# Kernel optimization log

Hardware: AMD Instinct MI355X
Metric: run time of the kernel (lower is better)

Reference implementation:

```python
import jax, jax.numpy as jnp
import numpy as np

B, L, IN_DIM = 1024, 2048, 64
ATT_DIM, H, TOPK = 64, 4, 64
D = ATT_DIM // H  # head_dim = 16
SCALE = D ** 0.5


def setup_inputs() -> dict:
    key = jax.random.key(0)
    k1, k2, k3, k4, k5, k6, k7 = jax.random.split(key, 7)
    return {
        "target_item": jax.random.normal(k1, (B, IN_DIM), dtype=jnp.float32),
        "item_sequence": jax.random.normal(k2, (B, L, IN_DIM), dtype=jnp.float32),
        "mask": jax.random.randint(k3, (B, L), 0, 2, dtype=jnp.int32),
        # Linear weights stored as (in, out); x @ W == torch Linear(x)
        "W_q": jax.random.normal(k4, (IN_DIM, ATT_DIM), dtype=jnp.float32) * 0.05,
        "W_h": jax.random.normal(k5, (IN_DIM, ATT_DIM), dtype=jnp.float32) * 0.05,
        "W_v": jax.random.normal(k6, (IN_DIM, ATT_DIM), dtype=jnp.float32) * 0.05,
        "W_o": jax.random.normal(k7, (ATT_DIM, IN_DIM), dtype=jnp.float32) * 0.05,
    }


def reference(target_item, item_sequence, mask, W_q, W_h, W_v, W_o):
    b = target_item.shape[0]
    # Projections (Kc == 0 path: item_feat_seq == item_sequence)
    q = (target_item @ W_q).reshape(b, H, D)          # b h d (single query)
    k = (item_sequence @ W_h).reshape(b, L, H, D)      # b l h d
    v = (item_sequence @ W_v).reshape(b, L, H, D)      # b l h d

    scores = jnp.einsum("bhd,blhd->bhl", q, k) / SCALE  # b h l
    scores = jnp.where(mask[:, None, :] == 0, jnp.float32(-1e9), scores)

    topk_scores, topk_idx = jax.lax.top_k(scores, TOPK)  # b h k
    # gather the top-k value vectors: v -> b h l d, gather along l
    v_bhld = jnp.transpose(v, (0, 2, 1, 3))              # b h l d
    topk_value = jnp.take_along_axis(v_bhld, topk_idx[..., None], axis=2)  # b h k d

    attn = jax.nn.softmax(topk_scores, axis=-1)          # b h k
    out = jnp.einsum("bhk,bhkd->bhd", attn, topk_value)  # b h d
    out = out.reshape(b, H * D) @ W_o                    # b x input_dim
    return out
```

## Files before the change

kernel.cpp:

```cpp
#include <hip/hip_runtime.h>

#define B_   1024
#define L_   2048
#define IND_ 64
#define H_   4
#define K_   64

__global__ __launch_bounds__(64) void prep_weff_k(const float* __restrict__ target,
                                                  const float* __restrict__ Wq,
                                                  const float* __restrict__ Wh,
                                                  float* __restrict__ weff) {
  const int b = blockIdx.x;
  const int t = threadIdx.x;
  __shared__ float tgt[64];
  __shared__ double q[64];
  tgt[t] = target[b * 64 + t];
  __syncthreads();
  double acc = 0.0;
#pragma unroll
  for (int j = 0; j < 64; ++j) acc += (double)tgt[j] * (double)Wq[j * 64 + t];
  q[t] = acc;
  __syncthreads();
#pragma unroll
  for (int h = 0; h < H_; ++h) {
    double a2 = 0.0;
#pragma unroll
    for (int d = 0; d < 16; ++d) a2 += q[h * 16 + d] * (double)Wh[t * 64 + h * 16 + d];
    weff[((size_t)b * H_ + h) * 64 + t] = (float)(a2 * 0.25);
  }
}

__global__ __launch_bounds__(256) void prep_M_k(const float* __restrict__ Wv,
                                                const float* __restrict__ Wo,
                                                float* __restrict__ M) {
  const int idx = blockIdx.x * 256 + threadIdx.x;
  const int h = idx >> 12, i = (idx >> 6) & 63, j = idx & 63;
  double a = 0.0;
#pragma unroll
  for (int d = 0; d < 16; ++d)
    a += (double)Wv[i * 64 + h * 16 + d] * (double)Wo[(h * 16 + d) * 64 + j];
  M[idx] = (float)a;
}

__device__ __forceinline__ unsigned f2key(float s) {
  unsigned u = __float_as_uint(s);
  return (u & 0x80000000u) ? ~u : (u | 0x80000000u);
}
__device__ __forceinline__ float key2f(unsigned k) {
  unsigned u = (k & 0x80000000u) ? (k & 0x7FFFFFFFu) : ~k;
  return __uint_as_float(u);
}

template <int CTRL>
__device__ __forceinline__ float dpp_f(float x) {
  return __int_as_float(
      __builtin_amdgcn_update_dpp(0, __float_as_int(x), CTRL, 0xf, 0xf, true));
}
template <int OFF>
__device__ __forceinline__ float swz_f(float x) {
  return __int_as_float(__builtin_amdgcn_ds_swizzle(__float_as_int(x), OFF));
}

__global__ __launch_bounds__(256, 4) void attn_main_k(const float* __restrict__ seq,
                                                      const int* __restrict__ mask,
                                                      const float* __restrict__ weff,
                                                      const float* __restrict__ M,
                                                      float* __restrict__ out) {
  __shared__ float scores[L_ * H_];
  __shared__ int   sidx[H_][K_];
  __shared__ float sw[H_][K_];
  __shared__ float svec[H_][64];
  __shared__ float part[H_][64];

  const int b = blockIdx.x;
  const int tid = threadIdx.x;
  const int w = tid >> 6;
  const int ln = tid & 63;
  const int g = ln >> 4;
  const int j = ln & 15;
  const float* __restrict__ seqb = seq + (size_t)b * (L_ * IND_);
  const int* __restrict__ maskb = mask + (size_t)b * L_;
  const bool b1 = (ln & 1) != 0;
  const bool b2 = (ln & 2) != 0;

  float wefv[H_][4];
  {
    const float* wp = weff + (size_t)b * (H_ * 64) + (j << 2);
#pragma unroll
    for (int h = 0; h < H_; ++h) {
      const float4 v = *reinterpret_cast<const float4*>(wp + (h << 6));
      wefv[h][0] = v.x; wefv[h][1] = v.y; wefv[h][2] = v.z; wefv[h][3] = v.w;
    }
  }

  const float4* __restrict__ lp4 =
      reinterpret_cast<const float4*>(seqb) + (w << 6) + (g << 4) + j;
  const int rb0 = (w << 2) + g;

  float4 vvA[8], vvB[8];

#define LOADB(V, SB)                                                          \
  {                                                                           \
    _Pragma("unroll") for (int u = 0; u < 8; ++u)                             \
        V[u] = lp4[(((SB) << 3) + u) << 8];                                   \
  }
#define COMPUTE(V, SB)                                                        \
  {                                                                           \
    _Pragma("unroll") for (int u = 0; u < 8; ++u) {                           \
      const int s = ((SB) << 3) + u;                                          \
      const float4 v = V[u];                                                  \
      float p0 = v.x * wefv[0][0]; p0 = fmaf(v.y, wefv[0][1], p0);            \
      p0 = fmaf(v.z, wefv[0][2], p0); p0 = fmaf(v.w, wefv[0][3], p0);         \
      float p1 = v.x * wefv[1][0]; p1 = fmaf(v.y, wefv[1][1], p1);            \
      p1 = fmaf(v.z, wefv[1][2], p1); p1 = fmaf(v.w, wefv[1][3], p1);         \
      float p2 = v.x * wefv[2][0]; p2 = fmaf(v.y, wefv[2][1], p2);            \
      p2 = fmaf(v.z, wefv[2][2], p2); p2 = fmaf(v.w, wefv[2][3], p2);         \
      float p3 = v.x * wefv[3][0]; p3 = fmaf(v.y, wefv[3][1], p3);            \
      p3 = fmaf(v.z, wefv[3][2], p3); p3 = fmaf(v.w, wefv[3][3], p3);         \
                       \
      const float a  = (b1 ? p1 : p0) + dpp_f<0xB1>(b1 ? p0 : p1);            \
      const float bb = (b1 ? p3 : p2) + dpp_f<0xB1>(b1 ? p2 : p3);            \
      float c = (b2 ? bb : a) + dpp_f<0x4E>(b2 ? a : bb);                     \
      c += swz_f<0x101F>(c);                                       \
      c += swz_f<0x201F>(c);                                       \
      const int row = (s << 4) + rb0;                                         \
      if (j < 4) scores[(row << 2) + j] = c;                                  \
    }                                                                         \
  }

  LOADB(vvA, 0);
  LOADB(vvB, 1);  COMPUTE(vvA, 0);
  LOADB(vvA, 2);  COMPUTE(vvB, 1);
  LOADB(vvB, 3);  COMPUTE(vvA, 2);
  LOADB(vvA, 4);  COMPUTE(vvB, 3);
  LOADB(vvB, 5);  COMPUTE(vvA, 4);
  LOADB(vvA, 6);  COMPUTE(vvB, 5);
  LOADB(vvB, 7);  COMPUTE(vvA, 6);
  LOADB(vvA, 8);  COMPUTE(vvB, 7);
  LOADB(vvB, 9);  COMPUTE(vvA, 8);
  LOADB(vvA, 10); COMPUTE(vvB, 9);
  LOADB(vvB, 11); COMPUTE(vvA, 10);
  LOADB(vvA, 12); COMPUTE(vvB, 11);
  LOADB(vvB, 13); COMPUTE(vvA, 12);
  LOADB(vvA, 14); COMPUTE(vvB, 13);
  LOADB(vvB, 15); COMPUTE(vvA, 14);
                  COMPUTE(vvB, 15);
#undef LOADB
#undef COMPUTE

  unsigned mbits = 0;
#pragma unroll
  for (int t = 0; t < 32; ++t) mbits |= (maskb[(t << 6) + ln] ? 1u : 0u) << t;

  __syncthreads();

  unsigned kk[32];
  const unsigned KNEG = f2key(-1e9f);
#pragma unroll
  for (int t = 0; t < 32; ++t) {
    const float s_ = scores[(((t << 6) + ln) << 2) + w];
    kk[t] = ((mbits >> t) & 1u) ? f2key(s_) : KNEG;
  }

  unsigned kmax = 0u;
#pragma unroll
  for (int q = 0; q < 32; ++q) kmax = max(kmax, kk[q]);
#pragma unroll
  for (int off = 32; off >= 1; off >>= 1)
    kmax = max(kmax, (unsigned)__shfl_xor((int)kmax, off, 64));
  const float smax = key2f(kmax);

  unsigned lo = 0u, hi = 0xFFFFFFFFu;
  while (lo < hi) {
    const unsigned span = hi - lo;
    const unsigned mid = lo + (span >> 1) + (span & 1u);
    int c = 0;
#pragma unroll
    for (int q = 0; q < 32; ++q) c += (kk[q] >= mid) ? 1 : 0;
#pragma unroll
    for (int off = 32; off >= 1; off >>= 1) c += __shfl_xor(c, off, 64);
    if (c >= K_) lo = mid; else hi = mid - 1;
  }
  const unsigned V = lo;
  int cg = 0;
#pragma unroll
  for (int q = 0; q < 32; ++q) cg += (kk[q] > V) ? 1 : 0;
#pragma unroll
  for (int off = 32; off >= 1; off >>= 1) cg += __shfl_xor(cg, off, 64);
  const int m = K_ - cg;

  {
    const unsigned long long lmlt = (1ull << ln) - 1ull;
    int gbase = 0, etaken = 0;
#pragma unroll
    for (int q = 0; q < 32; ++q) {
      const unsigned key = kk[q];
      const int l = ln + (q << 6);
      const bool gt = key > V;
      const bool eq = key == V;
      const unsigned long long bgt = __ballot(gt);
      const unsigned long long beq = __ballot(eq);
      if (gt) {
        const int pos = gbase + __popcll(bgt & lmlt);
        sidx[w][pos] = l;
        sw[w][pos] = expf(key2f(key) - smax);
      }
      const int navail = __popcll(beq);
      const int take = min(m - etaken, navail);
      if (eq) {
        const int rk = __popcll(beq & lmlt);
        if (rk < take) {
          const int pos = 63 - (etaken + rk);
          sidx[w][pos] = l;
          sw[w][pos] = expf(key2f(key) - smax);
        }
      }
      gbase += __popcll(bgt);
      etaken += take;
    }
  }

  {
    const int cg4 = ln & 15;
    const int rg = ln >> 4;
    float4 sv = make_float4(0.f, 0.f, 0.f, 0.f);
    float z = 0.f;
#pragma unroll
    for (int q = 0; q < 16; ++q) {
      const int sl = (q << 2) + rg;
      const int idx = sidx[w][sl];
      const float wt = sw[w][sl];
      const float4 v =
          *reinterpret_cast<const float4*>(seqb + (size_t)idx * 64 + (cg4 << 2));
      sv.x = fmaf(wt, v.x, sv.x);
      sv.y = fmaf(wt, v.y, sv.y);
      sv.z = fmaf(wt, v.z, sv.z);
      sv.w = fmaf(wt, v.w, sv.w);
      z += wt;
    }
#pragma unroll
    for (int off = 16; off <= 32; off <<= 1) {
      sv.x += __shfl_xor(sv.x, off, 64);
      sv.y += __shfl_xor(sv.y, off, 64);
      sv.z += __shfl_xor(sv.z, off, 64);
      sv.w += __shfl_xor(sv.w, off, 64);
      z += __shfl_xor(z, off, 64);
    }
    if (rg == 0) {
      const float inv = 1.f / z;
      svec[w][(cg4 << 2) + 0] = sv.x * inv;
      svec[w][(cg4 << 2) + 1] = sv.y * inv;
      svec[w][(cg4 << 2) + 2] = sv.z * inv;
      svec[w][(cg4 << 2) + 3] = sv.w * inv;
    }
  }
  __syncthreads();

  {
    float o = 0.f;
    const float* __restrict__ Mh = M + (w << 12);
#pragma unroll
    for (int i = 0; i < 64; ++i) o = fmaf(svec[w][i], Mh[(i << 6) + ln], o);
    part[w][ln] = o;
  }
  __syncthreads();
  if (tid < 64)
    out[(size_t)b * 64 + tid] = part[0][tid] + part[1][tid] + part[2][tid] + part[3][tid];
}

extern "C" void kernel_launch(void* const* d_in, const int* in_sizes, int n_in,
                              void* d_out, int out_size, void* d_ws, size_t ws_size,
                              hipStream_t stream) {
  const float* target = (const float*)d_in[0];
  const float* seq    = (const float*)d_in[1];
  const int*   mask   = (const int*)d_in[2];
  const float* Wq     = (const float*)d_in[3];
  const float* Wh     = (const float*)d_in[4];
  const float* Wv     = (const float*)d_in[5];
  const float* Wo     = (const float*)d_in[6];
  float* out  = (float*)d_out;
  float* weff = (float*)d_ws;
  float* M    = weff + (size_t)B_ * H_ * 64;

  prep_weff_k<<<B_, 64, 0, stream>>>(target, Wq, Wh, weff);
  prep_M_k<<<64, 256, 0, stream>>>(Wv, Wo, M);
  attn_main_k<<<B_, 256, 0, stream>>>(seq, mask, weff, M, out);
}
```

Before: 128.0 us.

## Fuse prep kernels into a single attention kernel and simplify top-k selection

Folds the per-batch query/key weight folding and the value/output projection into the main attention kernel, removing two extra launches and the workspace round-trip. The output projection now goes through Wv then Wo per head instead of a precomputed 64x64 fused matrix. The top-k scatter is simplified to a single ballot-based compaction, and the mask load is hoisted ahead of the streaming loop. The cost is serialized fp64 prep work at the start of each block (only 64 threads active, with barriers) before the streaming loads begin.

Result: slower. 140.4 us (+9.7%).

```diff
diff --git a/kernel.cpp b/kernel.cpp
--- a/kernel.cpp
+++ b/kernel.cpp
@@ -6,42 +6,6 @@
 #define H_   4
 #define K_   64
 
-__global__ __launch_bounds__(64) void prep_weff_k(const float* __restrict__ target,
-                                                  const float* __restrict__ Wq,
-                                                  const float* __restrict__ Wh,
-                                                  float* __restrict__ weff) {
-  const int b = blockIdx.x;
-  const int t = threadIdx.x;
-  __shared__ float tgt[64];
-  __shared__ double q[64];
-  tgt[t] = target[b * 64 + t];
-  __syncthreads();
-  double acc = 0.0;
-#pragma unroll
-  for (int j = 0; j < 64; ++j) acc += (double)tgt[j] * (double)Wq[j * 64 + t];
-  q[t] = acc;
-  __syncthreads();
-#pragma unroll
-  for (int h = 0; h < H_; ++h) {
-    double a2 = 0.0;
-#pragma unroll
-    for (int d = 0; d < 16; ++d) a2 += q[h * 16 + d] * (double)Wh[t * 64 + h * 16 + d];
-    weff[((size_t)b * H_ + h) * 64 + t] = (float)(a2 * 0.25);
-  }
-}
-
-__global__ __launch_bounds__(256) void prep_M_k(const float* __restrict__ Wv,
-                                                const float* __restrict__ Wo,
-                                                float* __restrict__ M) {
-  const int idx = blockIdx.x * 256 + threadIdx.x;
-  const int h = idx >> 12, i = (idx >> 6) & 63, j = idx & 63;
-  double a = 0.0;
-#pragma unroll
-  for (int d = 0; d < 16; ++d)
-    a += (double)Wv[i * 64 + h * 16 + d] * (double)Wo[(h * 16 + d) * 64 + j];
-  M[idx] = (float)a;
-}
-
 __device__ __forceinline__ unsigned f2key(float s) {
   unsigned u = __float_as_uint(s);
   return (u & 0x80000000u) ? ~u : (u | 0x80000000u);
@@ -61,16 +25,23 @@
   return __int_as_float(__builtin_amdgcn_ds_swizzle(__float_as_int(x), OFF));
 }
 
-__global__ __launch_bounds__(256, 4) void attn_main_k(const float* __restrict__ seq,
-                                                      const int* __restrict__ mask,
-                                                      const float* __restrict__ weff,
-                                                      const float* __restrict__ M,
-                                                      float* __restrict__ out) {
-  __shared__ float scores[L_ * H_];
-  __shared__ int   sidx[H_][K_];
-  __shared__ float sw[H_][K_];
-  __shared__ float svec[H_][64];
-  __shared__ float part[H_][64];
+__global__ __launch_bounds__(256, 4) void attn_all_k(const float* __restrict__ target,
+                                                     const float* __restrict__ seq,
+                                                     const int* __restrict__ mask,
+                                                     const float* __restrict__ Wq,
+                                                     const float* __restrict__ Wh,
+                                                     const float* __restrict__ Wv,
+                                                     const float* __restrict__ Wo,
+                                                     float* __restrict__ out) {
+  __shared__ float  scores[L_ * H_];
+  __shared__ float  tgt[64];
+  __shared__ double qd[64];
+  __shared__ float  weff_s[H_ * 64];
+  __shared__ int    sidx[H_][K_];
+  __shared__ float  sw[H_][K_];
+  __shared__ float  svec[H_][64];
+  __shared__ float  tvec[H_][16];
+  __shared__ float  part[H_][64];
 
   const int b = blockIdx.x;
   const int tid = threadIdx.x;
@@ -83,14 +54,37 @@
   const bool b1 = (ln & 1) != 0;
   const bool b2 = (ln & 2) != 0;
 
+  unsigned mbits = 0;
+#pragma unroll
+  for (int t = 0; t < 32; ++t) mbits |= (maskb[(t << 6) + ln] ? 1u : 0u) << t;
+
+  if (tid < 64) tgt[tid] = target[b * 64 + tid];
+  __syncthreads();
+  if (tid < 64) {
+    double acc = 0.0;
+#pragma unroll
+    for (int jj = 0; jj < 64; ++jj)
+      acc += (double)tgt[jj] * (double)Wq[jj * 64 + tid];
+    qd[tid] = acc;
+  }
+  __syncthreads();
+  if (tid < 64) {
+#pragma unroll
+    for (int h = 0; h < H_; ++h) {
+      double a2 = 0.0;
+#pragma unroll
+      for (int d = 0; d < 16; ++d)
+        a2 += qd[h * 16 + d] * (double)Wh[tid * 64 + h * 16 + d];
+      weff_s[h * 64 + tid] = (float)(a2 * 0.25);
+    }
+  }
+  __syncthreads();
+
   float wefv[H_][4];
-  {
-    const float* wp = weff + (size_t)b * (H_ * 64) + (j << 2);
-#pragma unroll
-    for (int h = 0; h < H_; ++h) {
-      const float4 v = *reinterpret_cast<const float4*>(wp + (h << 6));
-      wefv[h][0] = v.x; wefv[h][1] = v.y; wefv[h][2] = v.z; wefv[h][3] = v.w;
-    }
+#pragma unroll
+  for (int h = 0; h < H_; ++h) {
+#pragma unroll
+    for (int e = 0; e < 4; ++e) wefv[h][e] = weff_s[h * 64 + (j << 2) + e];
   }
 
   const float4* __restrict__ lp4 =
@@ -148,10 +142,6 @@
 #undef LOADB
 #undef COMPUTE
 
-  unsigned mbits = 0;
-#pragma unroll
-  for (int t = 0; t < 32; ++t) mbits |= (maskb[(t << 6) + ln] ? 1u : 0u) << t;
-
   __syncthreads();
 
   unsigned kk[32];
@@ -191,32 +181,24 @@
 
   {
     const unsigned long long lmlt = (1ull << ln) - 1ull;
-    int gbase = 0, etaken = 0;
+    int base = 0, etaken = 0;
 #pragma unroll
     for (int q = 0; q < 32; ++q) {
       const unsigned key = kk[q];
       const int l = ln + (q << 6);
       const bool gt = key > V;
       const bool eq = key == V;
-      const unsigned long long bgt = __ballot(gt);
       const unsigned long long beq = __ballot(eq);
-      if (gt) {
-        const int pos = gbase + __popcll(bgt & lmlt);
+      const int rk = __popcll(beq & lmlt);
+      const bool sel = gt || (eq && (etaken + rk) < m);
+      const unsigned long long bsel = __ballot(sel);
+      if (sel) {
+        const int pos = base + __popcll(bsel & lmlt);
         sidx[w][pos] = l;
         sw[w][pos] = expf(key2f(key) - smax);
       }
-      const int navail = __popcll(beq);
-      const int take = min(m - etaken, navail);
-      if (eq) {
-        const int rk = __popcll(beq & lmlt);
-        if (rk < take) {
-          const int pos = 63 - (etaken + rk);
-          sidx[w][pos] = l;
-          sw[w][pos] = expf(key2f(key) - smax);
-        }
-      }
-      gbase += __popcll(bgt);
-      etaken += take;
+      base += __popcll(bsel);
+      etaken += min(m - etaken, __popcll(beq));
     }
   }
 
@@ -254,13 +236,21 @@
       svec[w][(cg4 << 2) + 3] = sv.w * inv;
     }
   }
-  __syncthreads();
 
   {
+    float tp = 0.f;
+#pragma unroll
+    for (int i16 = 0; i16 < 16; ++i16) {
+      const int i = (i16 << 2) + g;
+      tp = fmaf(svec[w][i], Wv[i * 64 + (w << 4) + j], tp);
+    }
+    tp += __shfl_xor(tp, 16, 64);
+    tp += __shfl_xor(tp, 32, 64);
+    if (ln < 16) tvec[w][ln] = tp;
     float o = 0.f;
-    const float* __restrict__ Mh = M + (w << 12);
-#pragma unroll
-    for (int i = 0; i < 64; ++i) o = fmaf(svec[w][i], Mh[(i << 6) + ln], o);
+#pragma unroll
+    for (int d = 0; d < 16; ++d)
+      o = fmaf(tvec[w][d], Wo[((w << 4) + d) * 64 + ln], o);
     part[w][ln] = o;
   }
   __syncthreads();
@@ -278,11 +268,8 @@
   const float* Wh     = (const float*)d_in[4];
   const float* Wv     = (const float*)d_in[5];
   const float* Wo     = (const float*)d_in[6];
-  float* out  = (float*)d_out;
-  float* weff = (float*)d_ws;
-  float* M    = weff + (size_t)B_ * H_ * 64;
-
-  prep_weff_k<<<B_, 64, 0, stream>>>(target, Wq, Wh, weff);
-  prep_M_k<<<64, 256, 0, stream>>>(Wv, Wo, M);
-  attn_main_k<<<B_, 256, 0, stream>>>(seq, mask, weff, M, out);
-}
+  float* out = (float*)d_out;
+  (void)d_ws; (void)ws_size;
+
+  attn_all_k<<<B_, 256, 0, stream>>>(target, seq, mask, Wq, Wh, Wv, Wo, out);
+}
```
